# Performance work log

Hardware: AMD Instinct MI355X
Metric: run time of the kernel (lower is better)

The kernel has to match this reference:

```python
import jax, jax.numpy as jnp
import numpy as np


def setup_inputs() -> dict:
    key = jax.random.key(0)
    k_x, k_K, k_b, k_G = jax.random.split(key, 4)
    x = jax.random.normal(k_x, (12, 1), dtype=jnp.float32)
    K = jax.random.uniform(k_K, (4, 4), dtype=jnp.float32)
    b = jax.random.uniform(k_b, (4, 1), dtype=jnp.float32)
    G = jax.random.uniform(k_G, (4, 4), dtype=jnp.float32)
    adj = jnp.ones((4, 4), dtype=jnp.float32) - jnp.eye(4, dtype=jnp.float32)
    t = jnp.float32(0.0)
    return {"t": t, "x": x, "K": K, "b": b, "G": G, "adj": adj}


def reference(t, x, K, b, G, adj):
    # Symplectic-like structure matrix J (constant)
    J = jnp.array([[0., -1., 0., 0.],
                   [1., 0., 0., 0.],
                   [0., 0., 0., -1.],
                   [0., 0., 1., 0.]], dtype=x.dtype)
    # split state into angles x1, velocities x2, controller state xi (each (4,1))
    x1, x2, xi = x[:4], x[4:8], x[8:12]
    a = x1[:, 0]   # angles, shape (4,)
    v = x2[:, 0]   # velocities, shape (4,)
    # meshgrid semantics: angles_i[i,j] = a[i], angles_j[i,j] = a[j]
    g_ij = jnp.cos(a[None, :] - a[:, None])        # cos(theta_j - theta_i)
    x_ij = v[None, :] - v[:, None]                 # v_j - v_i
    interactions = (adj * g_ij * x_ij).sum(axis=0).reshape(4, 1)
    # dH/dxi = K^T tanh(K xi + b)
    dH = K.T @ jnp.tanh(K @ xi + b)
    u = -(adj * G).T @ dH
    dxdt = (5.0 / 4.0) * u * interactions
    # gamma = 0.1 * max eigenvalue of symmetric G G^T (real by construction)
    gamma = 0.1 * jnp.max(jnp.linalg.eigvalsh(G @ G.T))
    F = J - gamma * jnp.eye(4, dtype=x.dtype)
    dxi_dt = F @ dH + (adj * G) @ x2
    return jnp.concatenate((x2, dxdt, dxi_dt), axis=0)  # (12,1)
```

## Files before the change

kernel.cpp:

```cpp
#include <hip/hip_runtime.h>
#include <hip/hip_bf16.h>
#include <math.h>


__global__ void kuramoto_kernel(const float* __restrict__ x,
                                const float* __restrict__ K,
                                const float* __restrict__ b,
                                const float* __restrict__ G,
                                const float* __restrict__ adj,
                                float* __restrict__ out) {
    if (threadIdx.x != 0) return;

    float a[4], v[4], xi[4], Kr[16], br[4], Gr[16], adjr[16];
    #pragma unroll
    for (int i = 0; i < 4; ++i) {
        a[i]  = x[i];
        v[i]  = x[4 + i];
        xi[i] = x[8 + i];
        br[i] = b[i];
    }
    #pragma unroll
    for (int i = 0; i < 16; ++i) {
        Kr[i]   = K[i];
        Gr[i]   = G[i];
        adjr[i] = adj[i];
    }

    float th[4];
    #pragma unroll
    for (int i = 0; i < 4; ++i) {
        float s = br[i];
        #pragma unroll
        for (int j = 0; j < 4; ++j) s += Kr[i * 4 + j] * xi[j];
        th[i] = tanhf(s);
    }

    float dH[4];
    #pragma unroll
    for (int j = 0; j < 4; ++j) {
        float s = 0.0f;
        #pragma unroll
        for (int i = 0; i < 4; ++i) s += Kr[i * 4 + j] * th[i];
        dH[j] = s;
    }

    float inter[4];
    #pragma unroll
    for (int j = 0; j < 4; ++j) {
        float s = 0.0f;
        #pragma unroll
        for (int i = 0; i < 4; ++i)
            s += adjr[i * 4 + j] * cosf(a[j] - a[i]) * (v[j] - v[i]);
        inter[j] = s;
    }

    float u[4];
    #pragma unroll
    for (int j = 0; j < 4; ++j) {
        float s = 0.0f;
        #pragma unroll
        for (int i = 0; i < 4; ++i) s += adjr[i * 4 + j] * Gr[i * 4 + j] * dH[i];
        u[j] = -s;
    }

    float M[16];
    #pragma unroll
    for (int i = 0; i < 4; ++i) {
        #pragma unroll
        for (int j = 0; j < 4; ++j) {
            float s = 0.0f;
            #pragma unroll
            for (int k = 0; k < 4; ++k) s += Gr[i * 4 + k] * Gr[j * 4 + k];
            M[i * 4 + j] = s;
        }
    }

    float pv[4] = {1.0f, 1.0f, 1.0f, 1.0f};
    float lam = 0.0f;
    #pragma unroll
    for (int it = 0; it < 12; ++it) {
        float w[4];
        #pragma unroll
        for (int i = 0; i < 4; ++i) {
            float s = 0.0f;
            #pragma unroll
            for (int j = 0; j < 4; ++j) s += M[i * 4 + j] * pv[j];
            w[i] = s;
        }
        if (it == 11) {
            lam = pv[0]*w[0] + pv[1]*w[1] + pv[2]*w[2] + pv[3]*w[3];
        } else {
            float n2 = w[0]*w[0] + w[1]*w[1] + w[2]*w[2] + w[3]*w[3];
            float inv = rsqrtf(n2);
            #pragma unroll
            for (int i = 0; i < 4; ++i) pv[i] = w[i] * inv;
        }
    }
    float gamma = 0.1f * lam;

    float JdH[4] = { -dH[1], dH[0], -dH[3], dH[2] };

    float dxi[4];
    #pragma unroll
    for (int i = 0; i < 4; ++i) {
        float s = JdH[i] - gamma * dH[i];
        #pragma unroll
        for (int j = 0; j < 4; ++j) s += adjr[i * 4 + j] * Gr[i * 4 + j] * v[j];
        dxi[i] = s;
    }

    #pragma unroll
    for (int i = 0; i < 4; ++i) {
        out[i]     = v[i];
        out[4 + i] = 1.25f * u[i] * inter[i];
        out[8 + i] = dxi[i];
    }
}

extern "C" void kernel_launch(void* const* d_in, const int* in_sizes, int n_in,
                              void* d_out, int out_size, void* d_ws, size_t ws_size,
                              hipStream_t stream) {
    const float* x   = (const float*)d_in[1];
    const float* K   = (const float*)d_in[2];
    const float* b   = (const float*)d_in[3];
    const float* G   = (const float*)d_in[4];
    const float* adj = (const float*)d_in[5];
    float* out = (float*)d_out;

    kuramoto_kernel<<<dim3(1), dim3(64), 0, stream>>>(x, K, b, G, adj, out);
}
```

Measured before the change: 64.51 us.

## Vectorize input loads and use fast tanh/cos intrinsics with symmetry reuse

Loads inputs as float4 vectors, replaces tanhf and cosf with fast exp/cos intrinsics, computes each pairwise cosine once using symmetry, skips the diagonal terms, and builds only the lower triangle of G G^T. The goal is fewer instructions in a single-thread kernel whose runtime is dominated by launch overhead. The intrinsics lose some precision, and skipping i==j assumes the diagonal term is always zero, which holds because v_j - v_i is zero there.

```diff
diff --git a/kernel.cpp b/kernel.cpp
--- a/kernel.cpp
+++ b/kernel.cpp
@@ -1,7 +1,11 @@
 #include <hip/hip_runtime.h>
-#include <hip/hip_bf16.h>
 #include <math.h>
 
+
+__device__ __forceinline__ float fast_tanh(float s) {
+    float e = __expf(2.0f * s);
+    return 1.0f - __fdividef(2.0f, e + 1.0f);
+}
 
 __global__ void kuramoto_kernel(const float* __restrict__ x,
                                 const float* __restrict__ K,
@@ -11,20 +15,30 @@
                                 float* __restrict__ out) {
     if (threadIdx.x != 0) return;
 
-    float a[4], v[4], xi[4], Kr[16], br[4], Gr[16], adjr[16];
-    #pragma unroll
-    for (int i = 0; i < 4; ++i) {
-        a[i]  = x[i];
-        v[i]  = x[4 + i];
-        xi[i] = x[8 + i];
-        br[i] = b[i];
-    }
-    #pragma unroll
-    for (int i = 0; i < 16; ++i) {
-        Kr[i]   = K[i];
-        Gr[i]   = G[i];
-        adjr[i] = adj[i];
-    }
+    const float4* x4   = reinterpret_cast<const float4*>(x);
+    const float4* K4   = reinterpret_cast<const float4*>(K);
+    const float4* G4   = reinterpret_cast<const float4*>(G);
+    const float4* A4   = reinterpret_cast<const float4*>(adj);
+    const float4* b4   = reinterpret_cast<const float4*>(b);
+
+    float4 va  = x4[0];
+    float4 vv  = x4[1];
+    float4 vxi = x4[2];
+    float4 kr0 = K4[0], kr1 = K4[1], kr2 = K4[2], kr3 = K4[3];
+    float4 gr0 = G4[0], gr1 = G4[1], gr2 = G4[2], gr3 = G4[3];
+    float4 ar0 = A4[0], ar1 = A4[1], ar2 = A4[2], ar3 = A4[3];
+    float4 vb  = b4[0];
+
+    float a[4]  = { va.x, va.y, va.z, va.w };
+    float v[4]  = { vv.x, vv.y, vv.z, vv.w };
+    float xi[4] = { vxi.x, vxi.y, vxi.z, vxi.w };
+    float br[4] = { vb.x, vb.y, vb.z, vb.w };
+    float Kr[16] = { kr0.x,kr0.y,kr0.z,kr0.w, kr1.x,kr1.y,kr1.z,kr1.w,
+                     kr2.x,kr2.y,kr2.z,kr2.w, kr3.x,kr3.y,kr3.z,kr3.w };
+    float Gr[16] = { gr0.x,gr0.y,gr0.z,gr0.w, gr1.x,gr1.y,gr1.z,gr1.w,
+                     gr2.x,gr2.y,gr2.z,gr2.w, gr3.x,gr3.y,gr3.z,gr3.w };
+    float adjr[16] = { ar0.x,ar0.y,ar0.z,ar0.w, ar1.x,ar1.y,ar1.z,ar1.w,
+                       ar2.x,ar2.y,ar2.z,ar2.w, ar3.x,ar3.y,ar3.z,ar3.w };
 
     float th[4];
     #pragma unroll
@@ -32,7 +46,7 @@
         float s = br[i];
         #pragma unroll
         for (int j = 0; j < 4; ++j) s += Kr[i * 4 + j] * xi[j];
-        th[i] = tanhf(s);
+        th[i] = fast_tanh(s);
     }
 
     float dH[4];
@@ -44,13 +58,23 @@
         dH[j] = s;
     }
 
+    float c[4][4];
+    c[0][1] = c[1][0] = __cosf(a[1] - a[0]);
+    c[0][2] = c[2][0] = __cosf(a[2] - a[0]);
+    c[0][3] = c[3][0] = __cosf(a[3] - a[0]);
+    c[1][2] = c[2][1] = __cosf(a[2] - a[1]);
+    c[1][3] = c[3][1] = __cosf(a[3] - a[1]);
+    c[2][3] = c[3][2] = __cosf(a[3] - a[2]);
+
     float inter[4];
     #pragma unroll
     for (int j = 0; j < 4; ++j) {
         float s = 0.0f;
         #pragma unroll
-        for (int i = 0; i < 4; ++i)
-            s += adjr[i * 4 + j] * cosf(a[j] - a[i]) * (v[j] - v[i]);
+        for (int i = 0; i < 4; ++i) {
+            if (i != j)
+                s += adjr[i * 4 + j] * c[i][j] * (v[j] - v[i]);
+        }
         inter[j] = s;
     }
 
@@ -67,11 +91,12 @@
     #pragma unroll
     for (int i = 0; i < 4; ++i) {
         #pragma unroll
-        for (int j = 0; j < 4; ++j) {
+        for (int j = 0; j <= i; ++j) {
             float s = 0.0f;
             #pragma unroll
             for (int k = 0; k < 4; ++k) s += Gr[i * 4 + k] * Gr[j * 4 + k];
             M[i * 4 + j] = s;
+            M[j * 4 + i] = s;
         }
     }
 
```

After: 62.45 us. 3.2% less time.
